# Performance work log

Hardware: AMD Instinct MI355X
Metric: run time of the kernel (lower is better)

The kernel has to match this reference:

```python
import jax, jax.numpy as jnp
import numpy as np
from jax import lax

NUM_HEADS = 8
EPS = 1e-12  # torch F.normalize default eps


def setup_inputs() -> dict:
    key = jax.random.key(0)
    ks = jax.random.split(key, 7)
    B, C, H, W = 4, 128, 256, 256
    d = C // 2  # per-branch channels = 64
    x = jax.random.normal(ks[0], (B, C, H, W), jnp.float32)
    w_qkv1 = jax.random.normal(ks[1], (3 * d, d), jnp.float32) * 0.05
    w_qkv2 = jax.random.normal(ks[2], (3 * d, d), jnp.float32) * 0.05
    w_dw1 = jax.random.normal(ks[3], (3 * d, 1, 3, 3), jnp.float32) * 0.05
    w_dw2 = jax.random.normal(ks[4], (3 * d, 1, 3, 3), jnp.float32) * 0.05
    w_po1 = jax.random.normal(ks[5], (d, d), jnp.float32) * 0.05
    w_po2 = jax.random.normal(ks[6], (d, d), jnp.float32) * 0.05
    t1 = jnp.ones((NUM_HEADS, 1, 1), jnp.float32)
    t2 = jnp.ones((NUM_HEADS, 1, 1), jnp.float32)
    return {"x": x, "w_qkv1": w_qkv1, "w_qkv2": w_qkv2, "w_dw1": w_dw1,
            "w_dw2": w_dw2, "w_po1": w_po1, "w_po2": w_po2, "t1": t1, "t2": t2}


def _qkv(xb, w1x1, wdw):
    # 1x1 conv (pointwise) then 3x3 depthwise conv, no bias
    y = jnp.einsum('bchw,oc->bohw', xb, w1x1)
    y = lax.conv_general_dilated(
        y, wdw, window_strides=(1, 1), padding='SAME',
        dimension_numbers=('NCHW', 'OIHW', 'NCHW'),
        feature_group_count=y.shape[1])
    return y


def _heads(t, b, h, w):
    # b (head c) h w -> b head c (h*w)
    return t.reshape(b, NUM_HEADS, -1, h * w)


def _l2norm(t):
    n = jnp.sqrt(jnp.sum(t * t, axis=-1, keepdims=True))
    return t / jnp.maximum(n, EPS)


def reference(x, w_qkv1, w_qkv2, w_dw1, w_dw2, w_po1, w_po2, t1, t2):
    b, c, h, w = x.shape
    x1, x2 = jnp.split(x, 2, axis=1)
    q1, k1, v1 = jnp.split(_qkv(x1, w_qkv1, w_dw1), 3, axis=1)
    q2, k2, v2 = jnp.split(_qkv(x2, w_qkv2, w_dw2), 3, axis=1)
    q1, k1, v1 = (_heads(t, b, h, w) for t in (q1, k1, v1))
    q2, k2, v2 = (_heads(t, b, h, w) for t in (q2, k2, v2))
    q1, k1 = _l2norm(q1), _l2norm(k1)
    q2, k2 = _l2norm(q2), _l2norm(k2)
    # channel-wise attention: [b, head, c_h, c_h]
    attn1 = jax.nn.softmax(jnp.einsum('bhcn,bhdn->bhcd', q1, k1) * t1[None], axis=-1)
    attn2 = jax.nn.softmax(jnp.einsum('bhcn,bhdn->bhcd', q2, k2) * t2[None], axis=-1)
    # cross-branch V swap
    out1 = jnp.einsum('bhcd,bhdn->bhcn', attn1, v2).reshape(b, c // 2, h, w)
    out2 = jnp.einsum('bhcd,bhdn->bhcn', attn2, v1).reshape(b, c // 2, h, w)
    out1 = jnp.einsum('bchw,oc->bohw', out1, w_po1)
    out2 = jnp.einsum('bchw,oc->bohw', out2, w_po2)
    return jnp.concatenate([out1, out2], axis=1)
```

## Files before the change

### kernel.cpp

```cpp
#include <hip/hip_runtime.h>
#include <hip/hip_fp16.h>

#define NPIX 65536
#define WIMG 256
#define HIMG 256
#define TW 16
#define TH 8
#define HSTR 24
#define NSLOT 240
#define YCH 248

typedef __attribute__((ext_vector_type(8))) _Float16 half8;
typedef __attribute__((ext_vector_type(4))) float f32x4;

__device__ __forceinline__ unsigned int h2u(__half2 h) {
  union { __half2 h; unsigned int u; } c; c.h = h; return c.u;
}
__device__ __forceinline__ __half2 u2h(unsigned int u) {
  union { unsigned int u; __half2 h; } c; c.u = u; return c.h;
}
__device__ __forceinline__ __half2 sp2(_Float16 s) {
  union { _Float16 h[2]; __half2 v; } u; u.h[0] = s; u.h[1] = s; return u.v;
}
__device__ __forceinline__ int qk_idx(int ch, int pxblk) {
  return ch * 128 + ((pxblk ^ (ch & 7)) << 3);
}
__device__ __forceinline__ void ld16_lds(const void* g, void* l) {
  __builtin_amdgcn_global_load_lds(
      (const __attribute__((address_space(1))) unsigned int*)g,
      (__attribute__((address_space(3))) unsigned int*)l, 16, 0, 0);
}

__global__ void k_zero(float* __restrict__ p, int n) {
  int i = blockIdx.x * 256 + threadIdx.x;
  if (i < n) p[i] = 0.0f;
}

__global__ __launch_bounds__(256)
void k_wprep(const float* __restrict__ wq1, const float* __restrict__ wq2,
             const float* __restrict__ wd1, const float* __restrict__ wd2,
             _Float16* __restrict__ wqh, _Float16* __restrict__ wdh) {
  int i = blockIdx.x * 256 + threadIdx.x;
  if (i < 24576) {
    int br = i / 12288, j = i - br * 12288;
    wqh[i] = (_Float16)((br ? wq2 : wq1)[j]);
  } else if (i < 24576 + 6144) {
    int j = i - 24576;
    int br = j / 3072, r = j - br * 3072;
    int o = r >> 4, t = r & 15;
    wdh[j] = (t < 9) ? (_Float16)((br ? wd2 : wd1)[o * 9 + t]) : (_Float16)0.0f;
  }
}

__global__ __launch_bounds__(256)
void k_xt(const float* __restrict__ x, __half* __restrict__ xT) {
  __shared__ _Float16 tile[64 * 257];
  const int strip = blockIdx.x;
  const int br = blockIdx.y, b = blockIdx.z;
  const int tid = threadIdx.x;
  const float* xb = x + ((size_t)b * 128 + br * 64) * NPIX + strip * 256;
  #pragma unroll 8
  for (int c = 0; c < 64; ++c)
    tile[c * 257 + tid] = (_Float16)xb[(size_t)c * NPIX + tid];
  __syncthreads();
  __half* xo = xT + ((size_t)(b * 2 + br) * NPIX + strip * 256) * 64;
  const int j = tid & 7;
  #pragma unroll
  for (int i = 0; i < 8; ++i) {
    int p = (tid >> 3) + i * 32;
    half8 h;
    #pragma unroll
    for (int k = 0; k < 8; ++k) h[k] = tile[(j * 8 + k) * 257 + p];
    *(half8*)((_Float16*)xo + p * 64 + j * 8) = h;
  }
}

__global__ __launch_bounds__(256, 3)
void k_qkv(const __half* __restrict__ xT,
           const _Float16* __restrict__ wqh, const _Float16* __restrict__ wdh,
           const float* __restrict__ zpage,
           __half* __restrict__ vbuf, float* __restrict__ gram,
           float* __restrict__ sqq, float* __restrict__ sqk)
{
  __shared__ __align__(16) _Float16 xs[256 * 64];
  __shared__ __align__(16) _Float16 ys[32 * YCH];

  const int tid = threadIdx.x;
  const int lane = tid & 63;
  const int wid = tid >> 6;
  const int tile = blockIdx.x;
  const int br = blockIdx.y;
  const int b = blockIdx.z;
  const int tx0 = (tile & 15) * TW;
  const int ty0 = (tile >> 4) * TH;

  const _Float16* wqb = wqh + br * 12288;
  const _Float16* wdb = wdh + br * 3072;
  const __half* xTimg = xT + (size_t)(b * 2 + br) * NPIX * 64;

  {
    const int j = lane & 7, pl = lane >> 3;
    for (int it = wid; it < 30; it += 4) {
      int s = it * 8;
      int slot = s + pl;
      int hy = slot / HSTR;
      int hx = slot - hy * HSTR;
      int gy = ty0 - 1 + hy, gx = tx0 - 1 + hx;
      bool valid = (hx < 18) && ((unsigned)gy < HIMG) && ((unsigned)gx < WIMG);
      const void* src = valid
        ? (const void*)((const _Float16*)xTimg + (size_t)(gy * WIMG + gx) * 64
                        + ((j ^ (slot & 7)) << 3))
        : (const void*)((const char*)zpage + lane * 16);
      ld16_lds(src, (void*)(xs + s * 64));
    }
  }
  asm volatile("s_waitcnt vmcnt(0)" ::: "memory");
  __syncthreads();

  const int col = lane & 15;
  const int qrow = lane >> 4;
  const int oo = tid >> 3;
  const int row = tid & 7;

  unsigned int qreg[2][8], kreg[2][8];

  #pragma unroll
  for (int p = 0; p < 3; ++p) {
    #pragma unroll
    for (int h = 0; h < 2; ++h) {
      half8 wf[2][2];
      #pragma unroll
      for (int nt = 0; nt < 2; ++nt)
        #pragma unroll
        for (int kc = 0; kc < 2; ++kc)
          wf[kc][nt] = *(const half8*)(wqb
              + (((p * 64 + h * 32 + nt * 16 + col) << 6) + kc * 32 + qrow * 8));

      for (int mt = wid; mt < 15; mt += 4) {
        int px = mt * 16 + col;
        half8 af0 = *(const half8*)(xs + px * 64 + (((qrow    ) ^ (px & 7)) << 3));
        half8 af1 = *(const half8*)(xs + px * 64 + (((4 + qrow) ^ (px & 7)) << 3));
        f32x4 a0 = {0,0,0,0}, a1 = {0,0,0,0};
        a0 = __builtin_amdgcn_mfma_f32_16x16x32_f16(af0, wf[0][0], a0, 0, 0, 0);
        a0 = __builtin_amdgcn_mfma_f32_16x16x32_f16(af1, wf[1][0], a0, 0, 0, 0);
        a1 = __builtin_amdgcn_mfma_f32_16x16x32_f16(af0, wf[0][1], a1, 0, 0, 0);
        a1 = __builtin_amdgcn_mfma_f32_16x16x32_f16(af1, wf[1][1], a1, 0, 0, 0);
        int pxd = mt * 16 + qrow * 4;
        __half2* d0 = (__half2*)(ys + (col     ) * YCH + pxd);
        __half2* d1 = (__half2*)(ys + (col + 16) * YCH + pxd);
        d0[0] = __floats2half2_rn(a0[0], a0[1]);
        d0[1] = __floats2half2_rn(a0[2], a0[3]);
        d1[0] = __floats2half2_rn(a1[0], a1[1]);
        d1[1] = __floats2half2_rn(a1[2], a1[3]);
      }
      __syncthreads();

      {
        const int o = h * 32 + oo;
        const _Float16* wdp = wdb + ((p * 64 + o) << 4);
        half8 wv = *(const half8*)wdp;
        _Float16 w8v = wdp[8];
        __half2 w2[9];
        #pragma unroll
        for (int j = 0; j < 8; ++j) w2[j] = sp2(wv[j]);
        w2[8] = sp2(w8v);
        __half2 a[8];
        #pragma unroll
        for (int k2 = 0; k2 < 8; ++k2) a[k2] = u2h(0u);
        #pragma unroll
        for (int ky = 0; ky < 3; ++ky) {
          const _Float16* rp = ys + oo * YCH + (row + ky) * HSTR;
          uint4 ra = *(const uint4*)rp;
          uint4 rb = *(const uint4*)(rp + 8);
          unsigned int rc = *(const unsigned int*)(rp + 16);
          unsigned int A[9] = {ra.x, ra.y, ra.z, ra.w, rb.x, rb.y, rb.z, rb.w, rc};
          #pragma unroll
          for (int k2 = 0; k2 < 8; ++k2) {
            unsigned int M = (A[k2] >> 16) | (A[k2 + 1] << 16);
            a[k2] = __hfma2(w2[ky * 3 + 0], u2h(A[k2]), a[k2]);
            a[k2] = __hfma2(w2[ky * 3 + 1], u2h(M), a[k2]);
            a[k2] = __hfma2(w2[ky * 3 + 2], u2h(A[k2 + 1]), a[k2]);
          }
        }
        if (p == 0) {
          #pragma unroll
          for (int k2 = 0; k2 < 8; ++k2) qreg[h][k2] = h2u(a[k2]);
        } else if (p == 1) {
          #pragma unroll
          for (int k2 = 0; k2 < 8; ++k2) kreg[h][k2] = h2u(a[k2]);
        } else {
          __half* vrow = (__half*)(vbuf
              + ((size_t)((br * 4 + b) * 64 + o)) * NPIX
              + (ty0 + row) * WIMG + tx0);
          uint4 s0 = {h2u(a[0]), h2u(a[1]), h2u(a[2]), h2u(a[3])};
          uint4 s1 = {h2u(a[4]), h2u(a[5]), h2u(a[6]), h2u(a[7])};
          *(uint4*)vrow = s0;
          *(uint4*)(vrow + 8) = s1;
          if (h == 1) {
            _Float16* qsb = xs;
            _Float16* ksb = xs + 64 * 128;
            #pragma unroll
            for (int hh = 0; hh < 2; ++hh) {
              int ch = hh * 32 + oo;
              uint4 q0 = {qreg[hh][0], qreg[hh][1], qreg[hh][2], qreg[hh][3]};
              uint4 q1 = {qreg[hh][4], qreg[hh][5], qreg[hh][6], qreg[hh][7]};
              uint4 k0 = {kreg[hh][0], kreg[hh][1], kreg[hh][2], kreg[hh][3]};
              uint4 k1 = {kreg[hh][4], kreg[hh][5], kreg[hh][6], kreg[hh][7]};
              *(uint4*)(qsb + qk_idx(ch, 2 * row))     = q0;
              *(uint4*)(qsb + qk_idx(ch, 2 * row + 1)) = q1;
              *(uint4*)(ksb + qk_idx(ch, 2 * row))     = k0;
              *(uint4*)(ksb + qk_idx(ch, 2 * row + 1)) = k1;
            }
          }
        }
      }
      __syncthreads();
    }
  }

  {
    const _Float16* qsb = xs;
    const _Float16* ksb = xs + 64 * 128;
    f32x4 gqk = {0,0,0,0}, gqq = {0,0,0,0}, gkk = {0,0,0,0};
    int ch = wid * 16 + col;
    #pragma unroll
    for (int kc = 0; kc < 4; ++kc) {
      int pb = kc * 4 + qrow;
      half8 aq = *(const half8*)(qsb + qk_idx(ch, pb));
      half8 bk = *(const half8*)(ksb + qk_idx(ch, pb));
      gqk = __builtin_amdgcn_mfma_f32_16x16x32_f16(aq, bk, gqk, 0, 0, 0);
      gqq = __builtin_amdgcn_mfma_f32_16x16x32_f16(aq, aq, gqq, 0, 0, 0);
      gkk = __builtin_amdgcn_mfma_f32_16x16x32_f16(bk, bk, gkk, 0, 0, 0);
    }
    const int gb_off = (br * 4 + b);
    if (((lane >> 3) & 1) == (lane >> 5)) {
      float* gb = gram + gb_off * 512;
      int kch = ch;
      int qc0 = wid * 16 + qrow * 4;
      #pragma unroll
      for (int r = 0; r < 4; ++r) {
        int qch = qc0 + r;
        atomicAdd(&gb[(qch >> 3) * 64 + (qch & 7) * 8 + (kch & 7)], gqk[r]);
      }
    }
    if ((col >> 2) == qrow) {
      atomicAdd(&sqq[gb_off * 64 + ch], gqq[lane & 3]);
      atomicAdd(&sqk[gb_off * 64 + ch], gkk[lane & 3]);
    }
  }
}

__global__ __launch_bounds__(64)
void k_attn(const float* __restrict__ gram, const float* __restrict__ sqq,
            const float* __restrict__ sqk,
            const float* __restrict__ wpo1, const float* __restrict__ wpo2,
            const float* __restrict__ t1, const float* __restrict__ t2,
            float* __restrict__ weff)
{
  const int br = blockIdx.x, b = blockIdx.y;
  const int t = threadIdx.x;
  __shared__ float attn[8][8][8];
  const float* gb = gram + (br * 4 + b) * 512;
  const float* sq = sqq + (br * 4 + b) * 64;
  const float* sk = sqk + (br * 4 + b) * 64;
  const float* tt = br ? t2 : t1;
  {
    int h = t >> 3, cq = t & 7;
    float ts = tt[h];
    float qn = fmaxf(sqrtf(sq[h * 8 + cq]), 1e-12f);
    float lg[8], m = -1e30f;
    #pragma unroll
    for (int d2 = 0; d2 < 8; ++d2) {
      float kn = fmaxf(sqrtf(sk[h * 8 + d2]), 1e-12f);
      lg[d2] = ts * gb[h * 64 + cq * 8 + d2] / (qn * kn);
      m = fmaxf(m, lg[d2]);
    }
    float s = 0.f;
    #pragma unroll
    for (int d2 = 0; d2 < 8; ++d2) { lg[d2] = expf(lg[d2] - m); s += lg[d2]; }
    float inv = 1.0f / s;
    #pragma unroll
    for (int d2 = 0; d2 < 8; ++d2) attn[h][cq][d2] = lg[d2] * inv;
  }
  __syncthreads();
  const float* wpo = br ? wpo2 : wpo1;
  float* wb = weff + (br * 4 + b) * 4096;
  for (int cp = 0; cp < 64; ++cp) {
    int hp = cp >> 3, ip = cp & 7;
    float acc = 0.f;
    #pragma unroll
    for (int j = 0; j < 8; ++j)
      acc += wpo[t * 64 + hp * 8 + j] * attn[hp][j][ip];
    wb[cp * 64 + t] = acc;
  }
}

__global__ __launch_bounds__(256)
void k_out(const __half* __restrict__ vbuf, const float* __restrict__ weff,
           float* __restrict__ out)
{
  const int obr = blockIdx.y, b = blockIdx.z;
  const int px = blockIdx.x * 256 + threadIdx.x;
  const float* wb = weff + (obr * 4 + b) * 4096;
  const __half* vp = vbuf + ((size_t)((1 - obr) * 4 + b) * 64) * NPIX + px;
  float acc[64];
  #pragma unroll
  for (int o = 0; o < 64; ++o) acc[o] = 0.0f;
  for (int c = 0; c < 64; ++c) {
    float vc = __half2float(vp[(size_t)c * NPIX]);
    const float* wr = wb + c * 64;
    #pragma unroll
    for (int o = 0; o < 64; ++o) acc[o] = fmaf(wr[o], vc, acc[o]);
  }
  float* op = out + ((size_t)b * 128 + obr * 64) * NPIX + px;
  #pragma unroll
  for (int o = 0; o < 64; ++o) op[(size_t)o * NPIX] = acc[o];
}

extern "C" void kernel_launch(void* const* d_in, const int* in_sizes, int n_in,
                              void* d_out, int out_size, void* d_ws, size_t ws_size,
                              hipStream_t stream) {
  const float* x     = (const float*)d_in[0];
  const float* wqkv1 = (const float*)d_in[1];
  const float* wqkv2 = (const float*)d_in[2];
  const float* wdw1  = (const float*)d_in[3];
  const float* wdw2  = (const float*)d_in[4];
  const float* wpo1  = (const float*)d_in[5];
  const float* wpo2  = (const float*)d_in[6];
  const float* t1    = (const float*)d_in[7];
  const float* t2    = (const float*)d_in[8];

  char* ws = (char*)d_ws;
  __half* vbuf = (__half*)ws;
  float* gram  = (float*)(ws + 67108864);
  float* sqq   = gram + 4096;
  float* sqk   = sqq + 512;
  float* zpage = sqk + 512;
  float* weff  = zpage + 1024;
  _Float16* wqkvh = (_Float16*)(weff + 32768);
  _Float16* wdwh  = wqkvh + 24576;

  __half* xT = (__half*)d_out;

  k_zero<<<dim3(24), dim3(256), 0, stream>>>(gram, 6144);
  k_wprep<<<dim3(120), dim3(256), 0, stream>>>(wqkv1, wqkv2, wdw1, wdw2, wqkvh, wdwh);
  k_xt<<<dim3(256, 2, 4), dim3(256), 0, stream>>>(x, xT);
  k_qkv<<<dim3(512, 2, 4), dim3(256), 0, stream>>>(xT, wqkvh, wdwh,
                                                   zpage, vbuf, gram, sqq, sqk);
  k_attn<<<dim3(2, 4), dim3(64), 0, stream>>>(gram, sqq, sqk, wpo1, wpo2, t1, t2, weff);
  k_out<<<dim3(256, 2, 4), dim3(256), 0, stream>>>(vbuf, weff, (float*)d_out);
}
```

Before: 255.8 us.

## Double-buffer pointwise output to overlap MFMA stage with depthwise conv

```diff
diff --git a/kernel.cpp b/kernel.cpp
--- a/kernel.cpp
+++ b/kernel.cpp
@@ -75,7 +75,7 @@
   }
 }
 
-__global__ __launch_bounds__(256, 3)
+__global__ __launch_bounds__(256, 2)
 void k_qkv(const __half* __restrict__ xT,
            const _Float16* __restrict__ wqh, const _Float16* __restrict__ wdh,
            const float* __restrict__ zpage,
@@ -83,7 +83,7 @@
            float* __restrict__ sqq, float* __restrict__ sqk)
 {
   __shared__ __align__(16) _Float16 xs[256 * 64];
-  __shared__ __align__(16) _Float16 ys[32 * YCH];
+  __shared__ __align__(16) _Float16 ys[2 * 32 * YCH];
 
   const int tid = threadIdx.x;
   const int lane = tid & 63;
@@ -124,99 +124,103 @@
 
   unsigned int qreg[2][8], kreg[2][8];
 
-  #pragma unroll
-  for (int p = 0; p < 3; ++p) {
-    #pragma unroll
-    for (int h = 0; h < 2; ++h) {
-      half8 wf[2][2];
-      #pragma unroll
-      for (int nt = 0; nt < 2; ++nt)
-        #pragma unroll
-        for (int kc = 0; kc < 2; ++kc)
-          wf[kc][nt] = *(const half8*)(wqb
-              + (((p * 64 + h * 32 + nt * 16 + col) << 6) + kc * 32 + qrow * 8));
-
-      for (int mt = wid; mt < 15; mt += 4) {
-        int px = mt * 16 + col;
-        half8 af0 = *(const half8*)(xs + px * 64 + (((qrow    ) ^ (px & 7)) << 3));
-        half8 af1 = *(const half8*)(xs + px * 64 + (((4 + qrow) ^ (px & 7)) << 3));
-        f32x4 a0 = {0,0,0,0}, a1 = {0,0,0,0};
-        a0 = __builtin_amdgcn_mfma_f32_16x16x32_f16(af0, wf[0][0], a0, 0, 0, 0);
-        a0 = __builtin_amdgcn_mfma_f32_16x16x32_f16(af1, wf[1][0], a0, 0, 0, 0);
-        a1 = __builtin_amdgcn_mfma_f32_16x16x32_f16(af0, wf[0][1], a1, 0, 0, 0);
-        a1 = __builtin_amdgcn_mfma_f32_16x16x32_f16(af1, wf[1][1], a1, 0, 0, 0);
-        int pxd = mt * 16 + qrow * 4;
-        __half2* d0 = (__half2*)(ys + (col     ) * YCH + pxd);
-        __half2* d1 = (__half2*)(ys + (col + 16) * YCH + pxd);
-        d0[0] = __floats2half2_rn(a0[0], a0[1]);
-        d0[1] = __floats2half2_rn(a0[2], a0[3]);
-        d1[0] = __floats2half2_rn(a1[0], a1[1]);
-        d1[1] = __floats2half2_rn(a1[2], a1[3]);
-      }
-      __syncthreads();
-
-      {
-        const int o = h * 32 + oo;
-        const _Float16* wdp = wdb + ((p * 64 + o) << 4);
-        half8 wv = *(const half8*)wdp;
-        _Float16 w8v = wdp[8];
-        __half2 w2[9];
-        #pragma unroll
-        for (int j = 0; j < 8; ++j) w2[j] = sp2(wv[j]);
-        w2[8] = sp2(w8v);
-        __half2 a[8];
-        #pragma unroll
-        for (int k2 = 0; k2 < 8; ++k2) a[k2] = u2h(0u);
-        #pragma unroll
-        for (int ky = 0; ky < 3; ++ky) {
-          const _Float16* rp = ys + oo * YCH + (row + ky) * HSTR;
-          uint4 ra = *(const uint4*)rp;
-          uint4 rb = *(const uint4*)(rp + 8);
-          unsigned int rc = *(const unsigned int*)(rp + 16);
-          unsigned int A[9] = {ra.x, ra.y, ra.z, ra.w, rb.x, rb.y, rb.z, rb.w, rc};
-          #pragma unroll
-          for (int k2 = 0; k2 < 8; ++k2) {
-            unsigned int M = (A[k2] >> 16) | (A[k2 + 1] << 16);
-            a[k2] = __hfma2(w2[ky * 3 + 0], u2h(A[k2]), a[k2]);
-            a[k2] = __hfma2(w2[ky * 3 + 1], u2h(M), a[k2]);
-            a[k2] = __hfma2(w2[ky * 3 + 2], u2h(A[k2 + 1]), a[k2]);
-          }
-        }
-        if (p == 0) {
-          #pragma unroll
-          for (int k2 = 0; k2 < 8; ++k2) qreg[h][k2] = h2u(a[k2]);
-        } else if (p == 1) {
-          #pragma unroll
-          for (int k2 = 0; k2 < 8; ++k2) kreg[h][k2] = h2u(a[k2]);
-        } else {
-          __half* vrow = (__half*)(vbuf
-              + ((size_t)((br * 4 + b) * 64 + o)) * NPIX
-              + (ty0 + row) * WIMG + tx0);
-          uint4 s0 = {h2u(a[0]), h2u(a[1]), h2u(a[2]), h2u(a[3])};
-          uint4 s1 = {h2u(a[4]), h2u(a[5]), h2u(a[6]), h2u(a[7])};
-          *(uint4*)vrow = s0;
-          *(uint4*)(vrow + 8) = s1;
-          if (h == 1) {
-            _Float16* qsb = xs;
-            _Float16* ksb = xs + 64 * 128;
-            #pragma unroll
-            for (int hh = 0; hh < 2; ++hh) {
-              int ch = hh * 32 + oo;
-              uint4 q0 = {qreg[hh][0], qreg[hh][1], qreg[hh][2], qreg[hh][3]};
-              uint4 q1 = {qreg[hh][4], qreg[hh][5], qreg[hh][6], qreg[hh][7]};
-              uint4 k0 = {kreg[hh][0], kreg[hh][1], kreg[hh][2], kreg[hh][3]};
-              uint4 k1 = {kreg[hh][4], kreg[hh][5], kreg[hh][6], kreg[hh][7]};
-              *(uint4*)(qsb + qk_idx(ch, 2 * row))     = q0;
-              *(uint4*)(qsb + qk_idx(ch, 2 * row + 1)) = q1;
-              *(uint4*)(ksb + qk_idx(ch, 2 * row))     = k0;
-              *(uint4*)(ksb + qk_idx(ch, 2 * row + 1)) = k1;
-            }
-          }
-        }
-      }
-      __syncthreads();
-    }
-  }
+#define PW(S) do {                                                            \
+    const int p_ = (S) >> 1, h_ = (S) & 1;                                    \
+    _Float16* yb_ = ys + ((S) & 1) * 32 * YCH;                                \
+    half8 wf00 = *(const half8*)(wqb + (((p_ * 64 + h_ * 32 + col) << 6) + qrow * 8));            \
+    half8 wf10 = *(const half8*)(wqb + (((p_ * 64 + h_ * 32 + col) << 6) + 32 + qrow * 8));       \
+    half8 wf01 = *(const half8*)(wqb + (((p_ * 64 + h_ * 32 + 16 + col) << 6) + qrow * 8));       \
+    half8 wf11 = *(const half8*)(wqb + (((p_ * 64 + h_ * 32 + 16 + col) << 6) + 32 + qrow * 8));  \
+    for (int mt = wid; mt < 15; mt += 4) {                                    \
+      int px = mt * 16 + col;                                                 \
+      half8 af0 = *(const half8*)(xs + px * 64 + (((qrow    ) ^ (px & 7)) << 3)); \
+      half8 af1 = *(const half8*)(xs + px * 64 + (((4 + qrow) ^ (px & 7)) << 3)); \
+      f32x4 a0 = {0,0,0,0}, a1 = {0,0,0,0};                                   \
+      a0 = __builtin_amdgcn_mfma_f32_16x16x32_f16(af0, wf00, a0, 0, 0, 0);    \
+      a0 = __builtin_amdgcn_mfma_f32_16x16x32_f16(af1, wf10, a0, 0, 0, 0);    \
+      a1 = __builtin_amdgcn_mfma_f32_16x16x32_f16(af0, wf01, a1, 0, 0, 0);    \
+      a1 = __builtin_amdgcn_mfma_f32_16x16x32_f16(af1, wf11, a1, 0, 0, 0);    \
+      int pxd = mt * 16 + qrow * 4;                                           \
+      uint2 s0_ = {h2u(__floats2half2_rn(a0[0], a0[1])),                      \
+                   h2u(__floats2half2_rn(a0[2], a0[3]))};                     \
+      uint2 s1_ = {h2u(__floats2half2_rn(a1[0], a1[1])),                      \
+                   h2u(__floats2half2_rn(a1[2], a1[3]))};                     \
+      *(uint2*)(yb_ + (col     ) * YCH + pxd) = s0_;                          \
+      *(uint2*)(yb_ + (col + 16) * YCH + pxd) = s1_;                          \
+    }                                                                         \
+  } while (0)
+
+#define DW(S) do {                                                            \
+    const int p_ = (S) >> 1, h_ = (S) & 1;                                    \
+    const _Float16* yb_ = ys + ((S) & 1) * 32 * YCH;                          \
+    const int o_ = h_ * 32 + oo;                                              \
+    const _Float16* wdp_ = wdb + ((p_ * 64 + o_) << 4);                       \
+    half8 wv_ = *(const half8*)wdp_;                                          \
+    _Float16 w8_ = wdp_[8];                                                   \
+    __half2 w2_[9];                                                           \
+    _Pragma("unroll")                                                         \
+    for (int j = 0; j < 8; ++j) w2_[j] = sp2(wv_[j]);                         \
+    w2_[8] = sp2(w8_);                                                        \
+    __half2 a_[8];                                                            \
+    _Pragma("unroll")                                                         \
+    for (int k2 = 0; k2 < 8; ++k2) a_[k2] = u2h(0u);                          \
+    _Pragma("unroll")                                                         \
+    for (int ky = 0; ky < 3; ++ky) {                                          \
+      const _Float16* rp_ = yb_ + oo * YCH + (row + ky) * HSTR;               \
+      uint4 ra_ = *(const uint4*)rp_;                                         \
+      uint4 rb_ = *(const uint4*)(rp_ + 8);                                   \
+      unsigned int rc_ = *(const unsigned int*)(rp_ + 16);                    \
+      unsigned int A_[9] = {ra_.x, ra_.y, ra_.z, ra_.w,                       \
+                            rb_.x, rb_.y, rb_.z, rb_.w, rc_};                 \
+      _Pragma("unroll")                                                       \
+      for (int k2 = 0; k2 < 8; ++k2) {                                        \
+        unsigned int M_ = (A_[k2] >> 16) | (A_[k2 + 1] << 16);                \
+        a_[k2] = __hfma2(w2_[ky * 3 + 0], u2h(A_[k2]), a_[k2]);               \
+        a_[k2] = __hfma2(w2_[ky * 3 + 1], u2h(M_), a_[k2]);                   \
+        a_[k2] = __hfma2(w2_[ky * 3 + 2], u2h(A_[k2 + 1]), a_[k2]);           \
+      }                                                                       \
+    }                                                                         \
+    if (p_ == 0) {                                                            \
+      _Pragma("unroll")                                                       \
+      for (int k2 = 0; k2 < 8; ++k2) qreg[h_][k2] = h2u(a_[k2]);              \
+    } else if (p_ == 1) {                                                     \
+      _Pragma("unroll")                                                       \
+      for (int k2 = 0; k2 < 8; ++k2) kreg[h_][k2] = h2u(a_[k2]);              \
+    } else {                                                                  \
+      __half* vrow_ = (__half*)(vbuf                                          \
+          + ((size_t)((br * 4 + b) * 64 + o_)) * NPIX                         \
+          + (ty0 + row) * WIMG + tx0);                                        \
+      uint4 s0_ = {h2u(a_[0]), h2u(a_[1]), h2u(a_[2]), h2u(a_[3])};           \
+      uint4 s1_ = {h2u(a_[4]), h2u(a_[5]), h2u(a_[6]), h2u(a_[7])};           \
+      *(uint4*)vrow_ = s0_;                                                   \
+      *(uint4*)(vrow_ + 8) = s1_;                                             \
+    }                                                                         \
+  } while (0)
+
+  PW(0); __syncthreads();
+  PW(1); DW(0); __syncthreads();
+  PW(2); DW(1); __syncthreads();
+  PW(3); DW(2); __syncthreads();
+  PW(4); DW(3); __syncthreads();
+  PW(5); DW(4); __syncthreads();
+  DW(5);
+  {
+    _Float16* qsb = xs;
+    _Float16* ksb = xs + 64 * 128;
+    #pragma unroll
+    for (int hh = 0; hh < 2; ++hh) {
+      int ch = hh * 32 + oo;
+      uint4 q0 = {qreg[hh][0], qreg[hh][1], qreg[hh][2], qreg[hh][3]};
+      uint4 q1 = {qreg[hh][4], qreg[hh][5], qreg[hh][6], qreg[hh][7]};
+      uint4 k0 = {kreg[hh][0], kreg[hh][1], kreg[hh][2], kreg[hh][3]};
+      uint4 k1 = {kreg[hh][4], kreg[hh][5], kreg[hh][6], kreg[hh][7]};
+      *(uint4*)(qsb + qk_idx(ch, 2 * row))     = q0;
+      *(uint4*)(qsb + qk_idx(ch, 2 * row + 1)) = q1;
+      *(uint4*)(ksb + qk_idx(ch, 2 * row))     = k0;
+      *(uint4*)(ksb + qk_idx(ch, 2 * row + 1)) = k1;
+    }
+  }
+  __syncthreads();
 
   {
     const _Float16* qsb = xs;
@@ -248,6 +252,8 @@
       atomicAdd(&sqk[gb_off * 64 + ch], gkk[lane & 3]);
     }
   }
+#undef PW
+#undef DW
 }
 
 __global__ __launch_bounds__(64)
```

Result: slower. 279.6 us (+9.3%).

## Use MFMA for the output projection and merge zero/weight-prep kernels

Applied to the files above, without the earlier changes.

```diff
diff --git a/kernel.cpp b/kernel.cpp
--- a/kernel.cpp
+++ b/kernel.cpp
@@ -31,24 +31,25 @@
       (__attribute__((address_space(3))) unsigned int*)l, 16, 0, 0);
 }
 
-__global__ void k_zero(float* __restrict__ p, int n) {
+__global__ __launch_bounds__(256)
+void k_prep(const float* __restrict__ wq1, const float* __restrict__ wq2,
+            const float* __restrict__ wd1, const float* __restrict__ wd2,
+            float* __restrict__ zbuf,
+            _Float16* __restrict__ wqh, _Float16* __restrict__ wdh) {
   int i = blockIdx.x * 256 + threadIdx.x;
-  if (i < n) p[i] = 0.0f;
-}
-
-__global__ __launch_bounds__(256)
-void k_wprep(const float* __restrict__ wq1, const float* __restrict__ wq2,
-             const float* __restrict__ wd1, const float* __restrict__ wd2,
-             _Float16* __restrict__ wqh, _Float16* __restrict__ wdh) {
-  int i = blockIdx.x * 256 + threadIdx.x;
-  if (i < 24576) {
-    int br = i / 12288, j = i - br * 12288;
-    wqh[i] = (_Float16)((br ? wq2 : wq1)[j]);
-  } else if (i < 24576 + 6144) {
-    int j = i - 24576;
-    int br = j / 3072, r = j - br * 3072;
-    int o = r >> 4, t = r & 15;
-    wdh[j] = (t < 9) ? (_Float16)((br ? wd2 : wd1)[o * 9 + t]) : (_Float16)0.0f;
+  if (i < 6144) {
+    zbuf[i] = 0.0f;
+  } else {
+    int j = i - 6144;
+    if (j < 24576) {
+      int br = j / 12288, r = j - br * 12288;
+      wqh[j] = (_Float16)((br ? wq2 : wq1)[r]);
+    } else {
+      int k = j - 24576;
+      int br = k / 3072, r = k - br * 3072;
+      int o = r >> 4, t = r & 15;
+      wdh[k] = (t < 9) ? (_Float16)((br ? wd2 : wd1)[o * 9 + t]) : (_Float16)0.0f;
+    }
   }
 }
 
@@ -255,7 +256,7 @@
             const float* __restrict__ sqk,
             const float* __restrict__ wpo1, const float* __restrict__ wpo2,
             const float* __restrict__ t1, const float* __restrict__ t2,
-            float* __restrict__ weff)
+            _Float16* __restrict__ wefft)
 {
   const int br = blockIdx.x, b = blockIdx.y;
   const int t = threadIdx.x;
@@ -284,37 +285,85 @@
   }
   __syncthreads();
   const float* wpo = br ? wpo2 : wpo1;
-  float* wb = weff + (br * 4 + b) * 4096;
+  _Float16* wt = wefft + (br * 4 + b) * 4096;
   for (int cp = 0; cp < 64; ++cp) {
     int hp = cp >> 3, ip = cp & 7;
     float acc = 0.f;
     #pragma unroll
     for (int j = 0; j < 8; ++j)
       acc += wpo[t * 64 + hp * 8 + j] * attn[hp][j][ip];
-    wb[cp * 64 + t] = acc;
+    wt[t * 64 + cp] = (_Float16)acc;
   }
 }
 
 __global__ __launch_bounds__(256)
-void k_out(const __half* __restrict__ vbuf, const float* __restrict__ weff,
+void k_out(const __half* __restrict__ vbuf, const _Float16* __restrict__ wefft,
            float* __restrict__ out)
 {
+  __shared__ __align__(16) _Float16 vs[64 * 128];
+  __shared__ __align__(16) _Float16 vt[128 * 64];
+
+  const int strip = blockIdx.x;
   const int obr = blockIdx.y, b = blockIdx.z;
-  const int px = blockIdx.x * 256 + threadIdx.x;
-  const float* wb = weff + (obr * 4 + b) * 4096;
-  const __half* vp = vbuf + ((size_t)((1 - obr) * 4 + b) * 64) * NPIX + px;
-  float acc[64];
+  const int brv = 1 - obr;
+  const int tid = threadIdx.x;
+  const int lane = tid & 63;
+  const int wid = tid >> 6;
+  const int col = lane & 15;
+  const int qrow = lane >> 4;
+
+  const __half* vb = vbuf + ((size_t)(brv * 4 + b) * 64) * NPIX + strip * 128;
+
+  for (int i = 0; i < 4; ++i) {
+    int it = wid * 4 + i;
+    const void* src = (const void*)((const _Float16*)vb
+        + (size_t)(it * 4 + (lane >> 4)) * NPIX + (lane & 15) * 8);
+    ld16_lds(src, (void*)(vs + it * 512));
+  }
+  asm volatile("s_waitcnt vmcnt(0)" ::: "memory");
+  __syncthreads();
+
+  {
+    int px = tid & 127, cb = tid >> 7;
+    #pragma unroll
+    for (int j = 0; j < 4; ++j) {
+      half8 h;
+      #pragma unroll
+      for (int e = 0; e < 8; ++e) h[e] = vs[(cb * 32 + j * 8 + e) * 128 + px];
+      int chunk = cb * 4 + j;
+      *(half8*)(vt + ((px * 8 + (chunk ^ (px & 7))) << 3)) = h;
+    }
+  }
+  __syncthreads();
+
+  const _Float16* wt = wefft + (obr * 4 + b) * 4096;
+  half8 bf[2][4];
   #pragma unroll
-  for (int o = 0; o < 64; ++o) acc[o] = 0.0f;
-  for (int c = 0; c < 64; ++c) {
-    float vc = __half2float(vp[(size_t)c * NPIX]);
-    const float* wr = wb + c * 64;
-    #pragma unroll
-    for (int o = 0; o < 64; ++o) acc[o] = fmaf(wr[o], vc, acc[o]);
-  }
-  float* op = out + ((size_t)b * 128 + obr * 64) * NPIX + px;
+  for (int nt = 0; nt < 4; ++nt)
+    #pragma unroll
+    for (int kc = 0; kc < 2; ++kc)
+      bf[kc][nt] = *(const half8*)(wt + (nt * 16 + col) * 64 + kc * 32 + qrow * 8);
+
+  float* ob = out + ((size_t)b * 128 + obr * 64) * NPIX + strip * 128;
   #pragma unroll
-  for (int o = 0; o < 64; ++o) op[(size_t)o * NPIX] = acc[o];
+  for (int mi = 0; mi < 2; ++mi) {
+    int mt = wid * 2 + mi;
+    int px = mt * 16 + col;
+    half8 af0 = *(const half8*)(vt + ((px * 8 + ((qrow    ) ^ (px & 7))) << 3));
+    half8 af1 = *(const half8*)(vt + ((px * 8 + ((4 + qrow) ^ (px & 7))) << 3));
+    f32x4 acc[4] = {{0,0,0,0},{0,0,0,0},{0,0,0,0},{0,0,0,0}};
+    #pragma unroll
+    for (int nt = 0; nt < 4; ++nt) {
+      acc[nt] = __builtin_amdgcn_mfma_f32_16x16x32_f16(af0, bf[0][nt], acc[nt], 0, 0, 0);
+      acc[nt] = __builtin_amdgcn_mfma_f32_16x16x32_f16(af1, bf[1][nt], acc[nt], 0, 0, 0);
+    }
+    int pxd = mt * 16 + qrow * 4;
+    #pragma unroll
+    for (int nt = 0; nt < 4; ++nt) {
+      float4 s = {acc[nt][0], acc[nt][1], acc[nt][2], acc[nt][3]};
+      *(float4*)(ob + (size_t)(nt * 16 + col) * NPIX + pxd) = s;
+    }
+  }
 }
 
 extern "C" void kernel_launch(void* const* d_in, const int* in_sizes, int n_in,
@@ -336,17 +385,17 @@
   float* sqq   = gram + 4096;
   float* sqk   = sqq + 512;
   float* zpage = sqk + 512;
-  float* weff  = zpage + 1024;
-  _Float16* wqkvh = (_Float16*)(weff + 32768);
+  _Float16* wqkvh = (_Float16*)(zpage + 1024);
   _Float16* wdwh  = wqkvh + 24576;
+  _Float16* wefft = wdwh + 6144;
 
   __half* xT = (__half*)d_out;
 
-  k_zero<<<dim3(24), dim3(256), 0, stream>>>(gram, 6144);
-  k_wprep<<<dim3(120), dim3(256), 0, stream>>>(wqkv1, wqkv2, wdw1, wdw2, wqkvh, wdwh);
+  k_prep<<<dim3(144), dim3(256), 0, stream>>>(wqkv1, wqkv2, wdw1, wdw2,
+                                              gram, wqkvh, wdwh);
   k_xt<<<dim3(256, 2, 4), dim3(256), 0, stream>>>(x, xT);
   k_qkv<<<dim3(512, 2, 4), dim3(256), 0, stream>>>(xT, wqkvh, wdwh,
                                                    zpage, vbuf, gram, sqq, sqk);
-  k_attn<<<dim3(2, 4), dim3(64), 0, stream>>>(gram, sqq, sqk, wpo1, wpo2, t1, t2, weff);
-  k_out<<<dim3(256, 2, 4), dim3(256), 0, stream>>>(vbuf, weff, (float*)d_out);
-}
+  k_attn<<<dim3(2, 4), dim3(64), 0, stream>>>(gram, sqq, sqk, wpo1, wpo2, t1, t2, wefft);
+  k_out<<<dim3(512, 2, 4), dim3(256), 0, stream>>>(vbuf, wefft, (float*)d_out);
+}
```

New measurement: 226.6 us. 1.13x faster.
